# Kernel optimization log

Measured on AMD Instinct MI355X. Metric: run time of the kernel, lower is better.

Reference implementation:

```python
import jax, jax.numpy as jnp
import numpy as np

N = 10000   # num_nodes (batch=1)
E = 160000  # num edges
CIN, H, T, OUT, K = 32, 64, 12, 12, 3


def _conv1d(x, w, b, pad):
    # x: [N, C_in, T], w: [C_out, C_in, K]
    out = jax.lax.conv_general_dilated(
        x, w, window_strides=(1,), padding=[(pad, pad)],
        dimension_numbers=('NCH', 'OIH', 'NCH'))
    return out + b[None, :, None]


def _gated_tconv(x, w, b):
    # GatedTemporalConv (dropout = identity in eval)
    out = _conv1d(x, w, b, K // 2)
    P, Q = jnp.split(out, 2, axis=1)
    return P * jax.nn.sigmoid(Q)


def _gcn(x, W, b, src, dst, ew):
    # PyG GCNConv, vectorized over all T timesteps in one fused pass.
    # x: [N, C_in, T], W: [C_out, C_in]
    xt = jnp.einsum('nct,oc->not', x, W)
    loop = jnp.arange(N)
    srcl = jnp.concatenate([src, loop])
    dstl = jnp.concatenate([dst, loop])
    ewl = jnp.concatenate([ew, jnp.ones((N,), ew.dtype)])
    deg = jax.ops.segment_sum(ewl, dstl, num_segments=N)
    dis = jnp.where(deg > 0, jax.lax.rsqrt(deg), 0.0)
    norm = dis[srcl] * ewl * dis[dstl]                      # [E+N]
    msg = xt[srcl] * norm[:, None, None]                    # [E+N, C_out, T]
    out = jax.ops.segment_sum(msg, dstl, num_segments=N)    # [N, C_out, T]
    return out + b[None, :, None]


def setup_inputs() -> dict:
    key = jax.random.key(0)
    ks = jax.random.split(key, 20)
    rn = lambda k, s: jax.random.normal(k, s, jnp.float32) * 0.05
    return {
        'x': jax.random.normal(ks[0], (N, CIN, T), jnp.float32),
        'edge_index': jax.random.randint(ks[1], (2, E), 0, N),
        'edge_weight': jax.random.uniform(ks[2], (E,), jnp.float32),
        'tc1a_w': rn(ks[3], (2 * H, CIN, K)), 'tc1a_b': rn(ks[4], (2 * H,)),
        'gc1_w': rn(ks[5], (H, H)),           'gc1_b': rn(ks[6], (H,)),
        'tc1b_w': rn(ks[7], (2 * H, H, K)),   'tc1b_b': rn(ks[8], (2 * H,)),
        'tc2a_w': rn(ks[9], (2 * H, H, K)),   'tc2a_b': rn(ks[10], (2 * H,)),
        'gc2_w': rn(ks[11], (H, H)),          'gc2_b': rn(ks[12], (H,)),
        'tc2b_w': rn(ks[13], (2 * H, H, K)),  'tc2b_b': rn(ks[14], (2 * H,)),
        'fin_w': rn(ks[15], (OUT, H, T)),     'fin_b': rn(ks[16], (OUT,)),
    }


def reference(x, edge_index, edge_weight,
              tc1a_w, tc1a_b, gc1_w, gc1_b, tc1b_w, tc1b_b,
              tc2a_w, tc2a_b, gc2_w, gc2_b, tc2b_w, tc2b_b,
              fin_w, fin_b):
    src, dst = edge_index[0], edge_index[1]
    h = _gated_tconv(x, tc1a_w, tc1a_b)
    h = jax.nn.relu(_gcn(h, gc1_w, gc1_b, src, dst, edge_weight))
    h = _gated_tconv(h, tc1b_w, tc1b_b)
    h = _gated_tconv(h, tc2a_w, tc2a_b)
    h = jax.nn.relu(_gcn(h, gc2_w, gc2_b, src, dst, edge_weight))
    h = _gated_tconv(h, tc2b_w, tc2b_b)
    h = _conv1d(h, fin_w, fin_b, 0)          # [N, OUT, 1] (kernel == T)
    h = h[:, :, 0]                            # squeeze(-1)
    return h.reshape(1, N, OUT)               # batch_size = 1
```

## Files before the change

### kernel.cpp

```cpp
#include <hip/hip_runtime.h>
#include <hip/hip_bf16.h>
#include <stdint.h>

#define N_NODES 10000
#define N_EDGES 160000
#define BUCKET 128

typedef unsigned short u16;
typedef unsigned int u32;
typedef short s16v8 __attribute__((ext_vector_type(8)));
typedef float f32v4 __attribute__((ext_vector_type(4)));

__device__ __forceinline__ float bf2f(u16 v){ return __uint_as_float(((u32)v) << 16); }
__device__ __forceinline__ u16 f2bf(float f){
    u32 u = __float_as_uint(f);
    u32 r = (u + 0x7fffu + ((u >> 16) & 1u)) >> 16;
    return (u16)r;
}

struct SmallPtrs { const void* p[14]; };

__device__ __constant__ const int g_seg_off[15] = {
    0, 12288, 12416, 16512, 16576, 41152, 41280,
    65856, 65984, 70080, 70144, 94720, 94848, 104064, 104076
};
__device__ __constant__ const int g_seg_kind[14] = {
    1, 0, 0, 0, 2, 0, 2, 0, 0, 0, 2, 0, 0, 0
};

__global__ void k_convert_init(SmallPtrs ps, u16* __restrict__ dst,
                               float* deg, int* cur){
    int i = blockIdx.x * blockDim.x + threadIdx.x;
    if (i < 104076){
        int seg = 0, base = 0;
#pragma unroll
        for (int s = 0; s < 14; s++){
            if (i >= g_seg_off[s]){ seg = s; base = g_seg_off[s]; }
        }
        int li = i - base;
        float v = ((const float*)ps.p[seg])[li];
        int kind = g_seg_kind[seg];
        int dsto = li;
        if (kind){
            int CIN = (kind == 1) ? 32 : 64;
            int o = li / (3 * CIN);
            int rem = li - o * (3 * CIN);
            int c = rem / 3, d = rem - c * 3;
            dsto = d * 128 * CIN + o * CIN + c;
        }
        dst[base + dsto] = f2bf(v);
    }
    if (i < N_NODES){ deg[i] = 1.0f; cur[i] = 0; }
}

__launch_bounds__(256, 2)
__global__ void k_gconv_count(const float* __restrict__ xin, const u16* __restrict__ wg,
                              const u16* __restrict__ bg, u16* __restrict__ out,
                              const int* __restrict__ ei, const float* __restrict__ ew,
                              float* deg){
    if (blockIdx.x >= 1250){
        int e = (blockIdx.x - 1250) * 256 + threadIdx.x;
        if (e < N_EDGES){
            int d = ei[N_EDGES + e];
            atomicAdd(&deg[d], ew[e]);
        }
        return;
    }
    __shared__ __attribute__((aligned(16))) u16 xT[8][14][40];
    __shared__ __attribute__((aligned(16))) u16 Ho[8][12][72];
    int tid = threadIdx.x;
    int n0 = blockIdx.x * 8;

    int lane = tid & 63, wave = tid >> 6;
    int col = lane & 15, quad = lane >> 4;
    int o_p = wave * 16 + col, o_q = o_p + 64;

    s16v8 Bf[3][2];
#pragma unroll
    for (int pq = 0; pq < 2; pq++){
        int o = pq ? o_q : o_p;
#pragma unroll
        for (int d = 0; d < 3; d++)
            Bf[d][pq] = *(const s16v8*)(wg + d * 4096 + o * 32 + quad * 8);
    }

    for (int i = tid; i < 8 * 40; i += 256){
        int g = i / 40, c = i % 40;
        xT[g][0][c] = 0; xT[g][13][c] = 0;
    }
    {
        int g = tid >> 5, c = tid & 31;
        const float4* p = (const float4*)(xin + ((size_t)(n0 + g) * 32 + c) * 12);
        float4 v0 = p[0], v1 = p[1], v2 = p[2];
        xT[g][1][c] = f2bf(v0.x);  xT[g][2][c] = f2bf(v0.y);
        xT[g][3][c] = f2bf(v0.z);  xT[g][4][c] = f2bf(v0.w);
        xT[g][5][c] = f2bf(v1.x);  xT[g][6][c] = f2bf(v1.y);
        xT[g][7][c] = f2bf(v1.z);  xT[g][8][c] = f2bf(v1.w);
        xT[g][9][c] = f2bf(v2.x);  xT[g][10][c] = f2bf(v2.y);
        xT[g][11][c] = f2bf(v2.z); xT[g][12][c] = f2bf(v2.w);
    }
    __syncthreads();

    f32v4 aP[6], aQ[6];
#pragma unroll
    for (int mt = 0; mt < 6; mt++){ aP[mt] = (f32v4)0.f; aQ[mt] = (f32v4)0.f; }
#pragma unroll
    for (int mt = 0; mt < 6; mt++){
        int m = mt * 16 + col;
        int g = m / 12, t = m - 12 * g;
#pragma unroll
        for (int d = 0; d < 3; d++){
            s16v8 a = *(const s16v8*)&xT[g][t + d][quad * 8];
            aP[mt] = __builtin_amdgcn_mfma_f32_16x16x32_bf16(a, Bf[d][0], aP[mt], 0, 0, 0);
            aQ[mt] = __builtin_amdgcn_mfma_f32_16x16x32_bf16(a, Bf[d][1], aQ[mt], 0, 0, 0);
        }
    }
    float bP = bf2f(bg[o_p]), bQ = bf2f(bg[o_q]);
#pragma unroll
    for (int mt = 0; mt < 6; mt++){
#pragma unroll
        for (int r = 0; r < 4; r++){
            int m2 = mt * 16 + quad * 4 + r;
            int g = m2 / 12, t = m2 - 12 * g;
            float pv = aP[mt][r] + bP, qv = aQ[mt][r] + bQ;
            Ho[g][t][o_p] = f2bf(pv / (1.f + __expf(-qv)));
        }
    }
    __syncthreads();
    for (int i = tid; i < 768; i += 256){
        int g = i / 96, r = i % 96, t = r / 8, ch = r % 8;
        *(s16v8*)(out + (size_t)(n0 + g) * 768 + t * 64 + ch * 8) = *(const s16v8*)&Ho[g][t][ch * 8];
    }
}

__global__ void k_scatter(const int* __restrict__ ei, const float* __restrict__ ew,
                          const float* __restrict__ deg, int* cur, int2* __restrict__ epack){
    int e = blockIdx.x * blockDim.x + threadIdx.x;
    if (e < N_EDGES){
        int s = ei[e];
        int d = ei[N_EDGES + e];
        float nw = rsqrtf(deg[s]) * ew[e] * rsqrtf(deg[d]);
        int p = atomicAdd(&cur[d], 1);
        if (p < BUCKET) epack[d * BUCKET + p] = make_int2(s, __float_as_int(nw));
    }
}

__launch_bounds__(256, 6)
__global__ void k_gather(const u16* __restrict__ src, const float* __restrict__ deg,
                         const int* __restrict__ cur, const int2* __restrict__ ep,
                         u16* __restrict__ z){
    int slice = blockIdx.x & 7;
    int nb = blockIdx.x >> 3;
    int nl = threadIdx.x >> 3;
    int l8 = threadIdx.x & 7;
    int n = nb * 32 + nl;
    if (n >= N_NODES) return;
    int base = slice * 96 + l8 * 12;
    const u16* xr = src + (size_t)n * 768 + base;
    float sw = 1.0f / deg[n];
    float acc[12];
#pragma unroll
    for (int k = 0; k < 3; k++){
        ushort4 v = *(const ushort4*)(xr + k * 4);
        acc[k * 4 + 0] = sw * bf2f(v.x); acc[k * 4 + 1] = sw * bf2f(v.y);
        acc[k * 4 + 2] = sw * bf2f(v.z); acc[k * 4 + 3] = sw * bf2f(v.w);
    }
    int e = cur[n]; if (e > BUCKET) e = BUCKET;
    const int2* eb = ep + (size_t)n * BUCKET;
    int p = 0;
    for (; p + 1 < e; p += 2){
        int2 e0 = eb[p], e1 = eb[p + 1];
        float w0 = __int_as_float(e0.y), w1 = __int_as_float(e1.y);
        const u16* q0 = src + (size_t)e0.x * 768 + base;
        const u16* q1 = src + (size_t)e1.x * 768 + base;
        ushort4 a0 = *(const ushort4*)(q0);
        ushort4 a1 = *(const ushort4*)(q0 + 4);
        ushort4 a2 = *(const ushort4*)(q0 + 8);
        ushort4 c0 = *(const ushort4*)(q1);
        ushort4 c1 = *(const ushort4*)(q1 + 4);
        ushort4 c2 = *(const ushort4*)(q1 + 8);
        acc[0] = fmaf(w0, bf2f(a0.x), acc[0]); acc[1] = fmaf(w0, bf2f(a0.y), acc[1]);
        acc[2] = fmaf(w0, bf2f(a0.z), acc[2]); acc[3] = fmaf(w0, bf2f(a0.w), acc[3]);
        acc[4] = fmaf(w0, bf2f(a1.x), acc[4]); acc[5] = fmaf(w0, bf2f(a1.y), acc[5]);
        acc[6] = fmaf(w0, bf2f(a1.z), acc[6]); acc[7] = fmaf(w0, bf2f(a1.w), acc[7]);
        acc[8] = fmaf(w0, bf2f(a2.x), acc[8]); acc[9] = fmaf(w0, bf2f(a2.y), acc[9]);
        acc[10] = fmaf(w0, bf2f(a2.z), acc[10]); acc[11] = fmaf(w0, bf2f(a2.w), acc[11]);
        acc[0] = fmaf(w1, bf2f(c0.x), acc[0]); acc[1] = fmaf(w1, bf2f(c0.y), acc[1]);
        acc[2] = fmaf(w1, bf2f(c0.z), acc[2]); acc[3] = fmaf(w1, bf2f(c0.w), acc[3]);
        acc[4] = fmaf(w1, bf2f(c1.x), acc[4]); acc[5] = fmaf(w1, bf2f(c1.y), acc[5]);
        acc[6] = fmaf(w1, bf2f(c1.z), acc[6]); acc[7] = fmaf(w1, bf2f(c1.w), acc[7]);
        acc[8] = fmaf(w1, bf2f(c2.x), acc[8]); acc[9] = fmaf(w1, bf2f(c2.y), acc[9]);
        acc[10] = fmaf(w1, bf2f(c2.z), acc[10]); acc[11] = fmaf(w1, bf2f(c2.w), acc[11]);
    }
    if (p < e){
        int2 e0 = eb[p];
        float w0 = __int_as_float(e0.y);
        const u16* q0 = src + (size_t)e0.x * 768 + base;
#pragma unroll
        for (int k = 0; k < 3; k++){
            ushort4 v = *(const ushort4*)(q0 + k * 4);
            acc[k * 4 + 0] = fmaf(w0, bf2f(v.x), acc[k * 4 + 0]);
            acc[k * 4 + 1] = fmaf(w0, bf2f(v.y), acc[k * 4 + 1]);
            acc[k * 4 + 2] = fmaf(w0, bf2f(v.z), acc[k * 4 + 2]);
            acc[k * 4 + 3] = fmaf(w0, bf2f(v.w), acc[k * 4 + 3]);
        }
    }
    u16* zo = z + (size_t)n * 768 + base;
#pragma unroll
    for (int k = 0; k < 3; k++){
        ushort4 hv;
        hv.x = f2bf(acc[k * 4 + 0]); hv.y = f2bf(acc[k * 4 + 1]);
        hv.z = f2bf(acc[k * 4 + 2]); hv.w = f2bf(acc[k * 4 + 3]);
        *(ushort4*)(zo + k * 4) = hv;
    }
}

#define XIDX(g, row, c) (((g) * 14 + (row)) * 72 + (c))

template<bool LAST>
__launch_bounds__(256, 4)
__global__ void k_fused(const u16* __restrict__ z,
                        const u16* __restrict__ Wmix, const u16* __restrict__ bmix,
                        const u16* __restrict__ w1, const u16* __restrict__ b1,
                        const u16* __restrict__ w2, const u16* __restrict__ b2,
                        const u16* __restrict__ fw, const u16* __restrict__ fb,
                        u16* __restrict__ outMid, float* __restrict__ outFin){
    __shared__ __attribute__((aligned(16))) u16 bufX[4 * 14 * 72];
    __shared__ __attribute__((aligned(16))) u16 bufY[4 * 14 * 72];
    int tid = threadIdx.x;
    int n0 = blockIdx.x * 4;
    int lane = tid & 63, wave = tid >> 6;
    int col = lane & 15, quad = lane >> 4;
    int o_p = wave * 16 + col, o_q = o_p + 64;
    int o_mix = o_p;

    s16v8 Bm[2];
#pragma unroll
    for (int ks = 0; ks < 2; ks++)
        Bm[ks] = *(const s16v8*)(Wmix + (size_t)o_mix * 64 + ks * 32 + quad * 8);
    s16v8 Bf1[3][2][2];
#pragma unroll
    for (int pq = 0; pq < 2; pq++){
        int o = pq ? o_q : o_p;
#pragma unroll
        for (int d = 0; d < 3; d++)
#pragma unroll
            for (int ks = 0; ks < 2; ks++)
                Bf1[d][ks][pq] = *(const s16v8*)(w1 + d * 8192 + o * 64 + ks * 32 + quad * 8);
    }
    s16v8 Bf2[3][2][2];
    if (!LAST){
#pragma unroll
        for (int pq = 0; pq < 2; pq++){
            int o = pq ? o_q : o_p;
#pragma unroll
            for (int d = 0; d < 3; d++)
#pragma unroll
                for (int ks = 0; ks < 2; ks++)
                    Bf2[d][ks][pq] = *(const s16v8*)(w2 + d * 8192 + o * 64 + ks * 32 + quad * 8);
        }
    }
    float bmv = bf2f(bmix[o_mix]);
    float b1P = bf2f(b1[o_p]), b1Q = bf2f(b1[o_q]);
    float b2P = 0.f, b2Q = 0.f;
    if (!LAST){ b2P = bf2f(b2[o_p]); b2Q = bf2f(b2[o_q]); }

    for (int i = tid; i < 4 * 72; i += 256){
        int g = i / 72, c = i % 72;
        bufX[XIDX(g, 0, c)] = 0; bufX[XIDX(g, 13, c)] = 0;
        bufY[XIDX(g, 0, c)] = 0; bufY[XIDX(g, 13, c)] = 0;
    }
    for (int i = tid; i < 384; i += 256){
        int g = i / 96, r = i % 96, t = r >> 3, ch = r & 7;
        *(s16v8*)&bufX[XIDX(g, 1 + t, ch * 8)] =
            *(const s16v8*)(z + (size_t)(n0 + g) * 768 + t * 64 + ch * 8);
    }
    __syncthreads();

    {
        f32v4 accm[3];
#pragma unroll
        for (int mt = 0; mt < 3; mt++) accm[mt] = (f32v4)0.f;
#pragma unroll
        for (int mt = 0; mt < 3; mt++){
            int m = mt * 16 + col;
            int g = m / 12, t = m - 12 * g;
#pragma unroll
            for (int ks = 0; ks < 2; ks++){
                s16v8 a = *(const s16v8*)&bufX[XIDX(g, 1 + t, ks * 32 + quad * 8)];
                accm[mt] = __builtin_amdgcn_mfma_f32_16x16x32_bf16(a, Bm[ks], accm[mt], 0, 0, 0);
            }
        }
#pragma unroll
        for (int mt = 0; mt < 3; mt++){
#pragma unroll
            for (int r = 0; r < 4; r++){
                int m2 = mt * 16 + quad * 4 + r;
                int g = m2 / 12, t = m2 - 12 * g;
                bufY[XIDX(g, 1 + t, o_mix)] = f2bf(fmaxf(accm[mt][r] + bmv, 0.f));
            }
        }
    }
    __syncthreads();

    {
        f32v4 aP[3], aQ[3];
#pragma unroll
        for (int mt = 0; mt < 3; mt++){ aP[mt] = (f32v4)0.f; aQ[mt] = (f32v4)0.f; }
#pragma unroll
        for (int mt = 0; mt < 3; mt++){
            int m = mt * 16 + col;
            int g = m / 12, t = m - 12 * g;
#pragma unroll
            for (int d = 0; d < 3; d++)
#pragma unroll
                for (int ks = 0; ks < 2; ks++){
                    s16v8 a = *(const s16v8*)&bufY[XIDX(g, t + d, ks * 32 + quad * 8)];
                    aP[mt] = __builtin_amdgcn_mfma_f32_16x16x32_bf16(a, Bf1[d][ks][0], aP[mt], 0, 0, 0);
                    aQ[mt] = __builtin_amdgcn_mfma_f32_16x16x32_bf16(a, Bf1[d][ks][1], aQ[mt], 0, 0, 0);
                }
        }
#pragma unroll
        for (int mt = 0; mt < 3; mt++){
#pragma unroll
            for (int r = 0; r < 4; r++){
                int m2 = mt * 16 + quad * 4 + r;
                int g = m2 / 12, t = m2 - 12 * g;
                float pv = aP[mt][r] + b1P, qv = aQ[mt][r] + b1Q;
                u16 hv = f2bf(pv / (1.f + __expf(-qv)));
                if (LAST) bufX[g * 1008 + o_p * 12 + t] = hv;
                else      bufX[XIDX(g, 1 + t, o_p)] = hv;
            }
        }
    }
    __syncthreads();

    if (!LAST){
        f32v4 aP[3], aQ[3];
#pragma unroll
        for (int mt = 0; mt < 3; mt++){ aP[mt] = (f32v4)0.f; aQ[mt] = (f32v4)0.f; }
#pragma unroll
        for (int mt = 0; mt < 3; mt++){
            int m = mt * 16 + col;
            int g = m / 12, t = m - 12 * g;
#pragma unroll
            for (int d = 0; d < 3; d++)
#pragma unroll
                for (int ks = 0; ks < 2; ks++){
                    s16v8 a = *(const s16v8*)&bufX[XIDX(g, t + d, ks * 32 + quad * 8)];
                    aP[mt] = __builtin_amdgcn_mfma_f32_16x16x32_bf16(a, Bf2[d][ks][0], aP[mt], 0, 0, 0);
                    aQ[mt] = __builtin_amdgcn_mfma_f32_16x16x32_bf16(a, Bf2[d][ks][1], aQ[mt], 0, 0, 0);
                }
        }
#pragma unroll
        for (int mt = 0; mt < 3; mt++){
#pragma unroll
            for (int r = 0; r < 4; r++){
                int m2 = mt * 16 + quad * 4 + r;
                int g = m2 / 12, t = m2 - 12 * g;
                float pv = aP[mt][r] + b2P, qv = aQ[mt][r] + b2Q;
                bufY[XIDX(g, 1 + t, o_p)] = f2bf(pv / (1.f + __expf(-qv)));
            }
        }
        __syncthreads();
        for (int i = tid; i < 384; i += 256){
            int g = i / 96, r = i % 96, t = r / 8, ch = r % 8;
            *(s16v8*)(outMid + (size_t)(n0 + g) * 768 + t * 64 + ch * 8) =
                *(const s16v8*)&bufY[XIDX(g, 1 + t, ch * 8)];
        }
    } else {
        if (wave == 0){
            f32v4 accF = {0.f, 0.f, 0.f, 0.f};
            int g4 = col & 3;
#pragma unroll
            for (int ks = 0; ks < 24; ks++){
                s16v8 a = *(const s16v8*)&bufX[g4 * 1008 + ks * 32 + quad * 8];
                s16v8 bfr = {0, 0, 0, 0, 0, 0, 0, 0};
                if (col < 12)
                    bfr = *(const s16v8*)(fw + (size_t)col * 768 + ks * 32 + quad * 8);
                accF = __builtin_amdgcn_mfma_f32_16x16x32_bf16(a, bfr, accF, 0, 0, 0);
            }
            if (col < 12 && quad == 0){
                float bb = bf2f(fb[col]);
#pragma unroll
                for (int r = 0; r < 4; r++){
                    outFin[(size_t)(n0 + r) * 12 + col] = accF[r] + bb;
                }
            }
        }
    }
}

static inline size_t align256(size_t x){ return (x + 255) & ~(size_t)255; }

extern "C" void kernel_launch(void* const* d_in, const int* in_sizes, int n_in,
                              void* d_out, int out_size, void* d_ws, size_t ws_size,
                              hipStream_t stream){
    const float* x  = (const float*)d_in[0];
    const int* ei   = (const int*)d_in[1];
    const float* ew = (const float*)d_in[2];

    char* w = (char*)d_ws;
    u16* bufA    = (u16*)w;  w += align256((size_t)N_NODES * 768 * sizeof(u16));
    u16* bufB    = (u16*)w;  w += align256((size_t)N_NODES * 768 * sizeof(u16));
    u16* zA      = (u16*)w;  w += align256((size_t)N_NODES * 768 * sizeof(u16));
    u16* zB      = (u16*)w;  w += align256((size_t)N_NODES * 768 * sizeof(u16));
    float* deg   = (float*)w; w += align256(N_NODES * sizeof(float));
    int* cur     = (int*)w;   w += align256(N_NODES * sizeof(int));
    int2* epack  = (int2*)w;  w += align256((size_t)N_NODES * BUCKET * sizeof(int2));
    u16* cvt     = (u16*)w;   w += align256(104076 * sizeof(u16));

    u16* tc1a_w = cvt + 0;
    u16* tc1a_b = cvt + 12288;
    u16* gc1_w  = cvt + 12416;
    u16* gc1_b  = cvt + 16512;
    u16* tc1b_w = cvt + 16576;
    u16* tc1b_b = cvt + 41152;
    u16* tc2a_w = cvt + 41280;
    u16* tc2a_b = cvt + 65856;
    u16* gc2_w  = cvt + 65984;
    u16* gc2_b  = cvt + 70080;
    u16* tc2b_w = cvt + 70144;
    u16* tc2b_b = cvt + 94720;
    u16* fin_w  = cvt + 94848;
    u16* fin_b  = cvt + 104064;

    SmallPtrs ps;
    ps.p[0]  = d_in[3];  ps.p[1]  = d_in[4];
    ps.p[2]  = d_in[5];  ps.p[3]  = d_in[6];
    ps.p[4]  = d_in[7];  ps.p[5]  = d_in[8];
    ps.p[6]  = d_in[9];  ps.p[7]  = d_in[10];
    ps.p[8]  = d_in[11]; ps.p[9]  = d_in[12];
    ps.p[10] = d_in[13]; ps.p[11] = d_in[14];
    ps.p[12] = d_in[15]; ps.p[13] = d_in[16];

    k_convert_init<<<(104076 + 255) / 256, 256, 0, stream>>>(ps, cvt, deg, cur);
    k_gconv_count<<<1250 + 625, 256, 0, stream>>>(x, tc1a_w, tc1a_b, bufA, ei, ew, deg);
    k_scatter<<<625, 256, 0, stream>>>(ei, ew, deg, cur, epack);

    k_gather<<<313 * 8, 256, 0, stream>>>(bufA, deg, cur, epack, zA);
    k_fused<false><<<2500, 256, 0, stream>>>(zA, gc1_w, gc1_b, tc1b_w, tc1b_b,
                                             tc2a_w, tc2a_b, nullptr, nullptr,
                                             bufB, nullptr);
    k_gather<<<313 * 8, 256, 0, stream>>>(bufB, deg, cur, epack, zB);
    k_fused<true><<<2500, 256, 0, stream>>>(zB, gc2_w, gc2_b, tc2b_w, tc2b_b,
                                            nullptr, nullptr, fin_w, fin_b,
                                            nullptr, (float*)d_out);
}
```

Baseline: 261.6 us.

## Fold edge scatter into degree pass and double nodes per fused block

The separate scatter kernel is removed. Edge bucketing now happens in the degree-counting blocks and stores the raw edge weight, and the symmetric normalization (rsqrt of source and destination degree) is computed in the gather kernel. Separately, the fused GCN/temporal-conv kernel now handles 8 nodes per block instead of 4, with half the grid, and loads weights per k-slice instead of keeping them all in registers. This saves one launch and one pass over the edges, but adds a random deg[src] load per edge in each gather, and the bigger tiles double LDS use per block.

```diff
diff --git a/kernel.cpp b/kernel.cpp
--- a/kernel.cpp
+++ b/kernel.cpp
@@ -57,12 +57,16 @@
 __global__ void k_gconv_count(const float* __restrict__ xin, const u16* __restrict__ wg,
                               const u16* __restrict__ bg, u16* __restrict__ out,
                               const int* __restrict__ ei, const float* __restrict__ ew,
-                              float* deg){
+                              float* deg, int* cur, int2* __restrict__ epack){
     if (blockIdx.x >= 1250){
         int e = (blockIdx.x - 1250) * 256 + threadIdx.x;
         if (e < N_EDGES){
+            int s = ei[e];
             int d = ei[N_EDGES + e];
-            atomicAdd(&deg[d], ew[e]);
+            float wv = ew[e];
+            atomicAdd(&deg[d], wv);
+            int p = atomicAdd(&cur[d], 1);
+            if (p < BUCKET) epack[d * BUCKET + p] = make_int2(s, __float_as_int(wv));
         }
         return;
     }
@@ -130,18 +134,6 @@
     for (int i = tid; i < 768; i += 256){
         int g = i / 96, r = i % 96, t = r / 8, ch = r % 8;
         *(s16v8*)(out + (size_t)(n0 + g) * 768 + t * 64 + ch * 8) = *(const s16v8*)&Ho[g][t][ch * 8];
-    }
-}
-
-__global__ void k_scatter(const int* __restrict__ ei, const float* __restrict__ ew,
-                          const float* __restrict__ deg, int* cur, int2* __restrict__ epack){
-    int e = blockIdx.x * blockDim.x + threadIdx.x;
-    if (e < N_EDGES){
-        int s = ei[e];
-        int d = ei[N_EDGES + e];
-        float nw = rsqrtf(deg[s]) * ew[e] * rsqrtf(deg[d]);
-        int p = atomicAdd(&cur[d], 1);
-        if (p < BUCKET) epack[d * BUCKET + p] = make_int2(s, __float_as_int(nw));
     }
 }
 
@@ -157,7 +149,8 @@
     if (n >= N_NODES) return;
     int base = slice * 96 + l8 * 12;
     const u16* xr = src + (size_t)n * 768 + base;
-    float sw = 1.0f / deg[n];
+    float dn = rsqrtf(deg[n]);
+    float sw = dn * dn;
     float acc[12];
 #pragma unroll
     for (int k = 0; k < 3; k++){
@@ -170,7 +163,8 @@
     int p = 0;
     for (; p + 1 < e; p += 2){
         int2 e0 = eb[p], e1 = eb[p + 1];
-        float w0 = __int_as_float(e0.y), w1 = __int_as_float(e1.y);
+        float w0 = dn * __int_as_float(e0.y) * rsqrtf(deg[e0.x]);
+        float w1 = dn * __int_as_float(e1.y) * rsqrtf(deg[e1.x]);
         const u16* q0 = src + (size_t)e0.x * 768 + base;
         const u16* q1 = src + (size_t)e1.x * 768 + base;
         ushort4 a0 = *(const ushort4*)(q0);
@@ -194,7 +188,7 @@
     }
     if (p < e){
         int2 e0 = eb[p];
-        float w0 = __int_as_float(e0.y);
+        float w0 = dn * __int_as_float(e0.y) * rsqrtf(deg[e0.x]);
         const u16* q0 = src + (size_t)e0.x * 768 + base;
 #pragma unroll
         for (int k = 0; k < 3; k++){
@@ -225,52 +219,20 @@
                         const u16* __restrict__ w2, const u16* __restrict__ b2,
                         const u16* __restrict__ fw, const u16* __restrict__ fb,
                         u16* __restrict__ outMid, float* __restrict__ outFin){
-    __shared__ __attribute__((aligned(16))) u16 bufX[4 * 14 * 72];
-    __shared__ __attribute__((aligned(16))) u16 bufY[4 * 14 * 72];
+    __shared__ __attribute__((aligned(16))) u16 bufX[8 * 14 * 72];
+    __shared__ __attribute__((aligned(16))) u16 bufY[8 * 14 * 72];
     int tid = threadIdx.x;
-    int n0 = blockIdx.x * 4;
+    int n0 = blockIdx.x * 8;
     int lane = tid & 63, wave = tid >> 6;
     int col = lane & 15, quad = lane >> 4;
     int o_p = wave * 16 + col, o_q = o_p + 64;
-    int o_mix = o_p;
-
-    s16v8 Bm[2];
-#pragma unroll
-    for (int ks = 0; ks < 2; ks++)
-        Bm[ks] = *(const s16v8*)(Wmix + (size_t)o_mix * 64 + ks * 32 + quad * 8);
-    s16v8 Bf1[3][2][2];
-#pragma unroll
-    for (int pq = 0; pq < 2; pq++){
-        int o = pq ? o_q : o_p;
-#pragma unroll
-        for (int d = 0; d < 3; d++)
-#pragma unroll
-            for (int ks = 0; ks < 2; ks++)
-                Bf1[d][ks][pq] = *(const s16v8*)(w1 + d * 8192 + o * 64 + ks * 32 + quad * 8);
-    }
-    s16v8 Bf2[3][2][2];
-    if (!LAST){
-#pragma unroll
-        for (int pq = 0; pq < 2; pq++){
-            int o = pq ? o_q : o_p;
-#pragma unroll
-            for (int d = 0; d < 3; d++)
-#pragma unroll
-                for (int ks = 0; ks < 2; ks++)
-                    Bf2[d][ks][pq] = *(const s16v8*)(w2 + d * 8192 + o * 64 + ks * 32 + quad * 8);
-        }
-    }
-    float bmv = bf2f(bmix[o_mix]);
-    float b1P = bf2f(b1[o_p]), b1Q = bf2f(b1[o_q]);
-    float b2P = 0.f, b2Q = 0.f;
-    if (!LAST){ b2P = bf2f(b2[o_p]); b2Q = bf2f(b2[o_q]); }
-
-    for (int i = tid; i < 4 * 72; i += 256){
+
+    for (int i = tid; i < 8 * 72; i += 256){
         int g = i / 72, c = i % 72;
         bufX[XIDX(g, 0, c)] = 0; bufX[XIDX(g, 13, c)] = 0;
         bufY[XIDX(g, 0, c)] = 0; bufY[XIDX(g, 13, c)] = 0;
     }
-    for (int i = tid; i < 384; i += 256){
+    for (int i = tid; i < 768; i += 256){
         int g = i / 96, r = i % 96, t = r >> 3, ch = r & 7;
         *(s16v8*)&bufX[XIDX(g, 1 + t, ch * 8)] =
             *(const s16v8*)(z + (size_t)(n0 + g) * 768 + t * 64 + ch * 8);
@@ -278,55 +240,67 @@
     __syncthreads();
 
     {
-        f32v4 accm[3];
-#pragma unroll
-        for (int mt = 0; mt < 3; mt++) accm[mt] = (f32v4)0.f;
-#pragma unroll
-        for (int mt = 0; mt < 3; mt++){
-            int m = mt * 16 + col;
-            int g = m / 12, t = m - 12 * g;
-#pragma unroll
-            for (int ks = 0; ks < 2; ks++){
+        f32v4 accm[6];
+#pragma unroll
+        for (int mt = 0; mt < 6; mt++) accm[mt] = (f32v4)0.f;
+#pragma unroll
+        for (int ks = 0; ks < 2; ks++){
+            s16v8 Bm = *(const s16v8*)(Wmix + (size_t)o_p * 64 + ks * 32 + quad * 8);
+#pragma unroll
+            for (int mt = 0; mt < 6; mt++){
+                int m = mt * 16 + col;
+                int g = m / 12, t = m - 12 * g;
                 s16v8 a = *(const s16v8*)&bufX[XIDX(g, 1 + t, ks * 32 + quad * 8)];
-                accm[mt] = __builtin_amdgcn_mfma_f32_16x16x32_bf16(a, Bm[ks], accm[mt], 0, 0, 0);
-            }
-        }
-#pragma unroll
-        for (int mt = 0; mt < 3; mt++){
+                accm[mt] = __builtin_amdgcn_mfma_f32_16x16x32_bf16(a, Bm, accm[mt], 0, 0, 0);
+            }
+        }
+        float bm = bf2f(bmix[o_p]);
+#pragma unroll
+        for (int mt = 0; mt < 6; mt++){
 #pragma unroll
             for (int r = 0; r < 4; r++){
                 int m2 = mt * 16 + quad * 4 + r;
                 int g = m2 / 12, t = m2 - 12 * g;
-                bufY[XIDX(g, 1 + t, o_mix)] = f2bf(fmaxf(accm[mt][r] + bmv, 0.f));
+                bufY[XIDX(g, 1 + t, o_p)] = f2bf(fmaxf(accm[mt][r] + bm, 0.f));
             }
         }
     }
     __syncthreads();
 
     {
-        f32v4 aP[3], aQ[3];
-#pragma unroll
-        for (int mt = 0; mt < 3; mt++){ aP[mt] = (f32v4)0.f; aQ[mt] = (f32v4)0.f; }
-#pragma unroll
-        for (int mt = 0; mt < 3; mt++){
-            int m = mt * 16 + col;
-            int g = m / 12, t = m - 12 * g;
-#pragma unroll
-            for (int d = 0; d < 3; d++)
-#pragma unroll
-                for (int ks = 0; ks < 2; ks++){
+        f32v4 aP[6], aQ[6];
+#pragma unroll
+        for (int mt = 0; mt < 6; mt++){ aP[mt] = (f32v4)0.f; aQ[mt] = (f32v4)0.f; }
+#pragma unroll
+        for (int ks = 0; ks < 2; ks++){
+            s16v8 Bf[3][2];
+#pragma unroll
+            for (int pq = 0; pq < 2; pq++){
+                int o = pq ? o_q : o_p;
+#pragma unroll
+                for (int d = 0; d < 3; d++)
+                    Bf[d][pq] = *(const s16v8*)(w1 + d * 8192 + o * 64 + ks * 32 + quad * 8);
+            }
+#pragma unroll
+            for (int mt = 0; mt < 6; mt++){
+                int m = mt * 16 + col;
+                int g = m / 12, t = m - 12 * g;
+#pragma unroll
+                for (int d = 0; d < 3; d++){
                     s16v8 a = *(const s16v8*)&bufY[XIDX(g, t + d, ks * 32 + quad * 8)];
-                    aP[mt] = __builtin_amdgcn_mfma_f32_16x16x32_bf16(a, Bf1[d][ks][0], aP[mt], 0, 0, 0);
-                    aQ[mt] = __builtin_amdgcn_mfma_f32_16x16x32_bf16(a, Bf1[d][ks][1], aQ[mt], 0, 0, 0);
+                    aP[mt] = __builtin_amdgcn_mfma_f32_16x16x32_bf16(a, Bf[d][0], aP[mt], 0, 0, 0);
+                    aQ[mt] = __builtin_amdgcn_mfma_f32_16x16x32_bf16(a, Bf[d][1], aQ[mt], 0, 0, 0);
                 }
-        }
-#pragma unroll
-        for (int mt = 0; mt < 3; mt++){
+            }
+        }
+        float bP = bf2f(b1[o_p]), bQ = bf2f(b1[o_q]);
+#pragma unroll
+        for (int mt = 0; mt < 6; mt++){
 #pragma unroll
             for (int r = 0; r < 4; r++){
                 int m2 = mt * 16 + quad * 4 + r;
                 int g = m2 / 12, t = m2 - 12 * g;
-                float pv = aP[mt][r] + b1P, qv = aQ[mt][r] + b1Q;
+                float pv = aP[mt][r] + bP, qv = aQ[mt][r] + bQ;
                 u16 hv = f2bf(pv / (1.f + __expf(-qv)));
                 if (LAST) bufX[g * 1008 + o_p * 12 + t] = hv;
                 else      bufX[XIDX(g, 1 + t, o_p)] = hv;
@@ -336,34 +310,44 @@
     __syncthreads();
 
     if (!LAST){
-        f32v4 aP[3], aQ[3];
-#pragma unroll
-        for (int mt = 0; mt < 3; mt++){ aP[mt] = (f32v4)0.f; aQ[mt] = (f32v4)0.f; }
-#pragma unroll
-        for (int mt = 0; mt < 3; mt++){
-            int m = mt * 16 + col;
-            int g = m / 12, t = m - 12 * g;
-#pragma unroll
-            for (int d = 0; d < 3; d++)
-#pragma unroll
-                for (int ks = 0; ks < 2; ks++){
+        f32v4 aP[6], aQ[6];
+#pragma unroll
+        for (int mt = 0; mt < 6; mt++){ aP[mt] = (f32v4)0.f; aQ[mt] = (f32v4)0.f; }
+#pragma unroll
+        for (int ks = 0; ks < 2; ks++){
+            s16v8 Bf[3][2];
+#pragma unroll
+            for (int pq = 0; pq < 2; pq++){
+                int o = pq ? o_q : o_p;
+#pragma unroll
+                for (int d = 0; d < 3; d++)
+                    Bf[d][pq] = *(const s16v8*)(w2 + d * 8192 + o * 64 + ks * 32 + quad * 8);
+            }
+#pragma unroll
+            for (int mt = 0; mt < 6; mt++){
+                int m = mt * 16 + col;
+                int g = m / 12, t = m - 12 * g;
+#pragma unroll
+                for (int d = 0; d < 3; d++){
                     s16v8 a = *(const s16v8*)&bufX[XIDX(g, t + d, ks * 32 + quad * 8)];
-                    aP[mt] = __builtin_amdgcn_mfma_f32_16x16x32_bf16(a, Bf2[d][ks][0], aP[mt], 0, 0, 0);
-                    aQ[mt] = __builtin_amdgcn_mfma_f32_16x16x32_bf16(a, Bf2[d][ks][1], aQ[mt], 0, 0, 0);
+                    aP[mt] = __builtin_amdgcn_mfma_f32_16x16x32_bf16(a, Bf[d][0], aP[mt], 0, 0, 0);
+                    aQ[mt] = __builtin_amdgcn_mfma_f32_16x16x32_bf16(a, Bf[d][1], aQ[mt], 0, 0, 0);
                 }
-        }
-#pragma unroll
-        for (int mt = 0; mt < 3; mt++){
+            }
+        }
+        float bP = bf2f(b2[o_p]), bQ = bf2f(b2[o_q]);
+#pragma unroll
+        for (int mt = 0; mt < 6; mt++){
 #pragma unroll
             for (int r = 0; r < 4; r++){
                 int m2 = mt * 16 + quad * 4 + r;
                 int g = m2 / 12, t = m2 - 12 * g;
-                float pv = aP[mt][r] + b2P, qv = aQ[mt][r] + b2Q;
+                float pv = aP[mt][r] + bP, qv = aQ[mt][r] + bQ;
                 bufY[XIDX(g, 1 + t, o_p)] = f2bf(pv / (1.f + __expf(-qv)));
             }
         }
         __syncthreads();
-        for (int i = tid; i < 384; i += 256){
+        for (int i = tid; i < 768; i += 256){
             int g = i / 96, r = i % 96, t = r / 8, ch = r % 8;
             *(s16v8*)(outMid + (size_t)(n0 + g) * 768 + t * 64 + ch * 8) =
                 *(const s16v8*)&bufY[XIDX(g, 1 + t, ch * 8)];
@@ -371,20 +355,21 @@
     } else {
         if (wave == 0){
             f32v4 accF = {0.f, 0.f, 0.f, 0.f};
-            int g4 = col & 3;
+            int g8 = col & 7;
 #pragma unroll
             for (int ks = 0; ks < 24; ks++){
-                s16v8 a = *(const s16v8*)&bufX[g4 * 1008 + ks * 32 + quad * 8];
+                s16v8 a = *(const s16v8*)&bufX[g8 * 1008 + ks * 32 + quad * 8];
                 s16v8 bfr = {0, 0, 0, 0, 0, 0, 0, 0};
                 if (col < 12)
                     bfr = *(const s16v8*)(fw + (size_t)col * 768 + ks * 32 + quad * 8);
                 accF = __builtin_amdgcn_mfma_f32_16x16x32_bf16(a, bfr, accF, 0, 0, 0);
             }
-            if (col < 12 && quad == 0){
+            if (col < 12 && quad < 2){
                 float bb = bf2f(fb[col]);
 #pragma unroll
                 for (int r = 0; r < 4; r++){
-                    outFin[(size_t)(n0 + r) * 12 + col] = accF[r] + bb;
+                    int g = quad * 4 + r;
+                    outFin[(size_t)(n0 + g) * 12 + col] = accF[r] + bb;
                 }
             }
         }
@@ -435,15 +420,14 @@
     ps.p[12] = d_in[15]; ps.p[13] = d_in[16];
 
     k_convert_init<<<(104076 + 255) / 256, 256, 0, stream>>>(ps, cvt, deg, cur);
-    k_gconv_count<<<1250 + 625, 256, 0, stream>>>(x, tc1a_w, tc1a_b, bufA, ei, ew, deg);
-    k_scatter<<<625, 256, 0, stream>>>(ei, ew, deg, cur, epack);
+    k_gconv_count<<<1250 + 625, 256, 0, stream>>>(x, tc1a_w, tc1a_b, bufA, ei, ew, deg, cur, epack);
 
     k_gather<<<313 * 8, 256, 0, stream>>>(bufA, deg, cur, epack, zA);
-    k_fused<false><<<2500, 256, 0, stream>>>(zA, gc1_w, gc1_b, tc1b_w, tc1b_b,
+    k_fused<false><<<1250, 256, 0, stream>>>(zA, gc1_w, gc1_b, tc1b_w, tc1b_b,
                                              tc2a_w, tc2a_b, nullptr, nullptr,
                                              bufB, nullptr);
     k_gather<<<313 * 8, 256, 0, stream>>>(bufB, deg, cur, epack, zB);
-    k_fused<true><<<2500, 256, 0, stream>>>(zB, gc2_w, gc2_b, tc2b_w, tc2b_b,
+    k_fused<true><<<1250, 256, 0, stream>>>(zB, gc2_w, gc2_b, tc2b_w, tc2b_b,
                                             nullptr, nullptr, fin_w, fin_b,
                                             nullptr, (float*)d_out);
 }
```

Result: faster. 246.6 us (-5.7%).
